# Kernel optimization log

Hardware: AMD Instinct MI355X
Metric: run time of the kernel (lower is better)

The kernel has to match this reference:

```python
import jax, jax.numpy as jnp
import numpy as np

HEAD = 16

def setup_inputs() -> dict:
    key = jax.random.key(0)
    k1, k2, k3 = jax.random.split(key, 3)
    B, S, D = 2, 2048, 1024
    x = jax.random.normal(k1, (B, S, D), dtype=jnp.float32)
    w_qkv = jax.random.normal(k2, (D, 3 * D), dtype=jnp.float32) * (1.0 / np.sqrt(D))
    b_qkv = jnp.zeros((3 * D,), dtype=jnp.float32)
    w_out = jax.random.normal(k3, (D, D), dtype=jnp.float32) * (1.0 / np.sqrt(D))
    b_out = jnp.zeros((D,), dtype=jnp.float32)
    return {"x": x, "w_qkv": w_qkv, "b_qkv": b_qkv, "w_out": w_out, "b_out": b_out}


def reference(x, w_qkv, b_qkv, w_out, b_out):
    B, S, D = x.shape
    hd = D // HEAD  # head dim
    qkv = x @ w_qkv + b_qkv                      # [B,S,3D]
    qkv = qkv.reshape(B, S, 3, HEAD, hd)
    qkv = jnp.transpose(qkv, (2, 0, 3, 1, 4))    # [3,B,H,S,hd]
    q, k, v = qkv[0], qkv[1], qkv[2]
    scores = jnp.einsum('bhqd,bhkd->bhqk', q, k)  # [B,H,S,S]
    causal = jnp.triu(jnp.ones((S, S), dtype=bool), k=1)
    scores = jnp.where(causal, -jnp.inf, scores)
    scores = scores / jnp.sqrt(jnp.asarray(hd, dtype=x.dtype))
    attn = jax.nn.softmax(scores, axis=-1)
    z = jnp.einsum('bhqk,bhkd->bhqd', attn, v)   # [B,H,S,hd]
    z = jnp.transpose(z, (0, 2, 1, 3)).reshape(B, S, D)
    out = z @ w_out + b_out
    return out
```

## Files before the change

### kernel.cpp

```cpp
#include <hip/hip_runtime.h>

#define S_LEN  2048
#define NH     16
#define HD     64
#define DMODEL 1024

using bf16x8 = __attribute__((ext_vector_type(8))) __bf16;
using f32x4  = __attribute__((ext_vector_type(4))) float;

__device__ __forceinline__ unsigned short f2bf(float f) {
    unsigned u = __float_as_uint(f);
    u += 0x7FFFu + ((u >> 16) & 1u);
    return (unsigned short)(u >> 16);
}
__device__ __forceinline__ unsigned pk_trunc(float lo, float hi) {
    return __builtin_amdgcn_perm(__float_as_uint(hi), __float_as_uint(lo), 0x07060302u);
}

#define GLDS16(gsrc, ldst) \
    __builtin_amdgcn_global_load_lds((__attribute__((address_space(1))) void*)(gsrc), \
                                     (__attribute__((address_space(3))) void*)(ldst), 16, 0, 0)

#define WAIT_LGKM0() __builtin_amdgcn_s_waitcnt(0xC07F)

__global__ __launch_bounds__(256) void prep_kernel(
    const float* __restrict__ x, const float* __restrict__ w_qkv,
    const float* __restrict__ w_out,
    unsigned short* __restrict__ xb, unsigned short* __restrict__ wqkvT,
    unsigned short* __restrict__ woutT) {
    __shared__ float T[32][33];
    int bx = blockIdx.x;
    if (bx < 4096) {
        int idx = (bx * 256 + threadIdx.x) * 4;
        float4 v = *(const float4*)(x + idx);
        ushort4 o;
        o.x = f2bf(v.x); o.y = f2bf(v.y); o.z = f2bf(v.z); o.w = f2bf(v.w);
        *(ushort4*)(xb + idx) = o;
        return;
    }
    int tb = bx - 4096;
    int tcol = tb & 127, krow = tb >> 7;
    const float* in;
    unsigned short* out;
    int N, nbx;
    if (tcol < 96) { in = w_qkv; out = wqkvT; N = 3072; nbx = tcol; }
    else           { in = w_out; out = woutT; N = 1024; nbx = tcol - 96; }
    int r  = threadIdx.x >> 3;
    int c4 = (threadIdx.x & 7) * 4;
    int kbase = krow * 32, nbase = nbx * 32;
    float4 v = *(const float4*)(in + (size_t)(kbase + r) * N + nbase + c4);
    T[r][c4 + 0] = v.x; T[r][c4 + 1] = v.y; T[r][c4 + 2] = v.z; T[r][c4 + 3] = v.w;
    __syncthreads();
    ushort4 o;
    o.x = f2bf(T[c4 + 0][r]); o.y = f2bf(T[c4 + 1][r]);
    o.z = f2bf(T[c4 + 2][r]); o.w = f2bf(T[c4 + 3][r]);
    *(ushort4*)(out + (size_t)(nbase + r) * 1024 + kbase + c4) = o;
}

template <int NI>
__device__ __forceinline__ void mfma_mainloop64(const unsigned short* __restrict__ A,
                                                const unsigned short* __restrict__ B,
                                                int K, int m0, int n0,
                                                unsigned short* As, unsigned short* Bs,
                                                f32x4 acc[4][NI]) {
    const int lane = threadIdx.x & 63, wave = threadIdx.x >> 6;
    const int quad = lane >> 4, l15 = lane & 15;
    const int wm0 = (wave >> 1) * 64, wn0 = (wave & 1) * (NI * 16);

    for (int k0 = 0; k0 < K; k0 += 64) {
        __syncthreads();
        #pragma unroll
        for (int j = 0; j < 4 + NI; ++j) {
            if (j < 4) {
                int c0 = j * 256 + wave * 64;
                int c  = c0 + lane;
                int r = c >> 3, pc = c & 7, q = pc ^ (r & 7);
                GLDS16(A + (size_t)(m0 + r) * K + k0 + q * 8, As + c0 * 8);
            } else {
                int c0 = (j - 4) * 256 + wave * 64;
                int c  = c0 + lane;
                int r = c >> 3, pc = c & 7, q = pc ^ (r & 7);
                GLDS16(B + (size_t)(n0 + r) * K + k0 + q * 8, Bs + c0 * 8);
            }
        }
        __syncthreads();

        bf16x8 af[2][4], bfr[2][NI];
        #pragma unroll
        for (int mi = 0; mi < 4; ++mi) {
            int r = wm0 + mi * 16 + l15, x = r & 7;
            af[0][mi] = *(const bf16x8*)(As + r * 64 + ((quad    ) ^ x) * 8);
            af[1][mi] = *(const bf16x8*)(As + r * 64 + ((4 + quad) ^ x) * 8);
        }
        #pragma unroll
        for (int ni = 0; ni < NI; ++ni) {
            int r = wn0 + ni * 16 + l15, x = r & 7;
            bfr[0][ni] = *(const bf16x8*)(Bs + r * 64 + ((quad    ) ^ x) * 8);
            bfr[1][ni] = *(const bf16x8*)(Bs + r * 64 + ((4 + quad) ^ x) * 8);
        }
        #pragma unroll
        for (int h = 0; h < 2; ++h)
            #pragma unroll
            for (int mi = 0; mi < 4; ++mi)
                #pragma unroll
                for (int ni = 0; ni < NI; ++ni)
                    acc[mi][ni] = __builtin_amdgcn_mfma_f32_16x16x32_bf16(
                        af[h][mi], bfr[h][ni], acc[mi][ni], 0, 0, 0);
    }
}

__global__ __launch_bounds__(256) void gemm_qkv_kernel(
    const unsigned short* __restrict__ xb, const unsigned short* __restrict__ wT,
    const float* __restrict__ bias,
    unsigned short* __restrict__ Qt, unsigned short* __restrict__ Kh,
    unsigned short* __restrict__ Vt) {
    __shared__ __align__(16) unsigned short Sh[16384];
    unsigned short* As = Sh;
    unsigned short* Bs = Sh + 8192;

    f32x4 acc[4][4];
    #pragma unroll
    for (int i = 0; i < 4; ++i)
        #pragma unroll
        for (int j = 0; j < 4; ++j) acc[i][j] = (f32x4){0.f, 0.f, 0.f, 0.f};

    const int bid = blockIdx.x;
    const int xcd = bid & 7, slot = bid >> 3;
    const int nt = xcd * 3 + (slot % 3);
    const int mt = slot / 3;
    const int m0 = mt * 128, n0 = nt * 128;
    mfma_mainloop64<4>(xb, wT, DMODEL, m0, n0, As, Bs, acc);

    const int lane = threadIdx.x & 63, wave = threadIdx.x >> 6;
    const int quad = lane >> 4, l15 = lane & 15;
    const int wm0 = (wave >> 1) * 64, wn0 = (wave & 1) * 64;

    const int colbase = n0 + wn0;
    const int t = colbase >> 10;
    const int h = (colbase >> 6) & (NH - 1);
    const float qscale = (t == 0) ? 0.125f * 1.44269504088896f : 1.0f;
    float bv[4];
    #pragma unroll
    for (int ni = 0; ni < 4; ++ni) bv[ni] = bias[colbase + ni * 16 + l15];

    __syncthreads();
    unsigned short* Lw = Sh + wave * 1536;

    #pragma unroll
    for (int mi = 0; mi < 4; ++mi) {
        int mbase = m0 + wm0 + mi * 16;
        int b = mbase >> 11, sbase = mbase & (S_LEN - 1);
        if (t == 1) {
            #pragma unroll
            for (int ni = 0; ni < 4; ++ni)
                #pragma unroll
                for (int r = 0; r < 4; ++r)
                    Lw[(quad * 4 + r) * 72 + ni * 16 + l15] =
                        f2bf(acc[mi][ni][r] + bv[ni]);
            WAIT_LGKM0();
            int rr = lane & 15, dc = (lane >> 4) * 16;
            uint4 v0 = *(const uint4*)(Lw + rr * 72 + dc);
            uint4 v1 = *(const uint4*)(Lw + rr * 72 + dc + 8);
            unsigned short* dst =
                Kh + ((size_t)(b * NH + h) * S_LEN + sbase + rr) * HD + dc;
            *(uint4*)dst = v0;
            *(uint4*)(dst + 8) = v1;
        } else {
            #pragma unroll
            for (int ni = 0; ni < 4; ++ni)
                #pragma unroll
                for (int r = 0; r < 4; ++r)
                    Lw[(ni * 16 + l15) * 24 + quad * 4 + r] =
                        f2bf((acc[mi][ni][r] + bv[ni]) * qscale);
            WAIT_LGKM0();
            int c = lane;
            uint4 v0 = *(const uint4*)(Lw + c * 24);
            uint4 v1 = *(const uint4*)(Lw + c * 24 + 8);
            unsigned short* base = (t == 0) ? Qt : Vt;
            unsigned short* dst =
                base + ((size_t)(b * NH + h) * HD + c) * S_LEN + sbase;
            *(uint4*)dst = v0;
            *(uint4*)(dst + 8) = v1;
        }
        WAIT_LGKM0();
    }
}

__global__ __launch_bounds__(256) void gemm_out_kernel(
    const unsigned short* __restrict__ zb, const unsigned short* __restrict__ wT,
    const float* __restrict__ bias, float* __restrict__ out) {
    __shared__ __align__(16) unsigned short As[8192], Bs[4096];
    f32x4 acc[4][2];
    #pragma unroll
    for (int i = 0; i < 4; ++i)
        #pragma unroll
        for (int j = 0; j < 2; ++j) acc[i][j] = (f32x4){0.f, 0.f, 0.f, 0.f};

    const int bid = blockIdx.x;
    const int xcd = bid & 7, slot = bid >> 3;
    const int nt = xcd * 2 + (slot & 1);
    const int mt = slot >> 1;
    const int m0 = mt * 128, n0 = nt * 64;
    mfma_mainloop64<2>(zb, wT, DMODEL, m0, n0, As, Bs, acc);

    const int lane = threadIdx.x & 63, wave = threadIdx.x >> 6;
    const int quad = lane >> 4, l15 = lane & 15;
    const int wm0 = (wave >> 1) * 64, wn0 = (wave & 1) * 32;
    #pragma unroll
    for (int mi = 0; mi < 4; ++mi) {
        #pragma unroll
        for (int ni = 0; ni < 2; ++ni) {
            int col = n0 + wn0 + ni * 16 + l15;
            float bvv = bias[col];
            #pragma unroll
            for (int r = 0; r < 4; ++r)
                out[(size_t)(m0 + wm0 + mi * 16 + quad * 4 + r) * DMODEL + col] =
                    acc[mi][ni][r] + bvv;
        }
    }
}

__device__ const int g_sched[47 * 4] = {
    16,0,16,-1,
    31,0,15,0,  31,16,31,1,  30,0,15,0,  15,0,15,-1,
    30,16,30,1, 29,0,14,0,   29,15,29,1, 28,0,14,0,  14,0,14,-1,
    28,15,28,1, 27,0,13,0,   27,14,27,1, 26,0,13,0,  13,0,13,-1,
    26,14,26,1, 25,0,12,0,   25,13,25,1, 24,0,12,0,  12,0,12,-1,
    24,13,24,1, 23,0,11,0,   23,12,23,1, 22,0,11,0,  11,0,11,-1,
    22,12,22,1, 21,0,10,0,   21,11,21,1, 20,0,10,0,  10,0,10,-1,
    20,11,20,1, 19,0,9,0,    19,10,19,1, 18,0,9,0,   9,0,9,-1,
    18,10,18,1, 17,0,8,0,    17,9,17,1,  8,0,8,-1,
    7,0,7,-1, 6,0,6,-1, 5,0,5,-1, 4,0,4,-1, 3,0,3,-1, 2,0,2,-1, 1,0,1,-1, 0,0,0,-1
};

__global__ __launch_bounds__(256) void attn_mfma_kernel(
    const unsigned short* __restrict__ Qt, const unsigned short* __restrict__ Kh,
    const unsigned short* __restrict__ Vt, unsigned short* __restrict__ zb,
    float* __restrict__ Zp, float* __restrict__ lp) {
    __shared__ __align__(16) unsigned short Ks[64 * 64];
    __shared__ __align__(16) unsigned short Vs[64 * 64];
    __shared__ __align__(16) unsigned short Pl[4 * 16 * 64];

    const int lane = threadIdx.x & 63, wave = threadIdx.x >> 6;
    const int quad = lane >> 4, l15 = lane & 15;
    const int bh = blockIdx.x;
    const int qt   = g_sched[blockIdx.y * 4 + 0];
    const int klo  = g_sched[blockIdx.y * 4 + 1];
    const int khi  = g_sched[blockIdx.y * 4 + 2];
    const int part = g_sched[blockIdx.y * 4 + 3];
    const int q0 = qt * 64;
    const float M0 = 12.0f;

    bf16x8 qf0, qf1;
    {
        const unsigned short* qb = Qt + (size_t)bh * HD * S_LEN + q0 + wave * 16 + l15;
        union { bf16x8 v; unsigned short u[8]; } u0, u1;
        #pragma unroll
        for (int j = 0; j < 8; ++j) {
            u0.u[j] = qb[(quad * 8 + j) * S_LEN];
            u1.u[j] = qb[(32 + quad * 8 + j) * S_LEN];
        }
        qf0 = u0.v; qf1 = u1.v;
    }

    f32x4 Z[4];
    #pragma unroll
    for (int i = 0; i < 4; ++i) Z[i] = (f32x4){0.f, 0.f, 0.f, 0.f};
    float rsum = 0.f;

    unsigned short* pw = Pl + wave * 1024;
    const int pwrow = l15 * 64;
    const int qthr  = wave * 16 + l15 - quad * 4;

    for (int kt = klo; kt <= khi; ++kt) {
        __syncthreads();
        #pragma unroll
        for (int i = 0; i < 2; ++i) {
            int c0 = (i * 4 + wave) * 64;
            int c  = c0 + lane;
            int r = c >> 3, pc = c & 7, q = pc ^ (r & 7);
            GLDS16(Kh + ((size_t)bh * S_LEN + kt * 64 + r) * HD + q * 8, Ks + c0 * 8);
        }
        #pragma unroll
        for (int i = 0; i < 2; ++i) {
            int c0 = (i * 4 + wave) * 64;
            int c  = c0 + lane;
            int d = c >> 3, pc = c & 7, q = pc ^ (d & 7);
            GLDS16(Vt + ((size_t)bh * HD + d) * S_LEN + kt * 64 + q * 8, Vs + c0 * 8);
        }
        __syncthreads();

        const bool diag = (kt == qt);
        const int nmax = diag ? wave : 3;

        #pragma unroll
        for (int n = 0; n < 4; ++n) {
            int woff = pwrow + (((2 * n + (quad >> 1)) ^ (l15 & 7)) << 3) + (quad & 1) * 4;
            if (n <= nmax) {
                int rk = n * 16 + l15;
                int x = rk & 7;
                bf16x8 kv0 = *(const bf16x8*)(Ks + rk * 64 + ((quad    ) ^ x) * 8);
                bf16x8 kv1 = *(const bf16x8*)(Ks + rk * 64 + ((4 + quad) ^ x) * 8);
                f32x4 t4 = (f32x4){-M0, -M0, -M0, -M0};
                t4 = __builtin_amdgcn_mfma_f32_16x16x32_bf16(kv0, qf0, t4, 0, 0, 0);
                t4 = __builtin_amdgcn_mfma_f32_16x16x32_bf16(kv1, qf1, t4, 0, 0, 0);
                float p[4];
                #pragma unroll
                for (int r = 0; r < 4; ++r) {
                    p[r] = exp2f(t4[r]);
                    if (diag && (n * 16 + r) > qthr) p[r] = 0.f;
                    rsum += p[r];
                }
                uint2 pk;
                pk.x = pk_trunc(p[0], p[1]);
                pk.y = pk_trunc(p[2], p[3]);
                *(uint2*)(pw + woff) = pk;
            } else {
                *(uint2*)(pw + woff) = (uint2){0u, 0u};
            }
        }

        const int khmax = diag ? (wave >> 1) : 1;
        for (int kh = 0; kh <= khmax; ++kh) {
            bf16x8 pa = *(const bf16x8*)(pw + pwrow + ((kh * 4 + quad) ^ (l15 & 7)) * 8);
            #pragma unroll
            for (int ni = 0; ni < 4; ++ni) {
                int rd = ni * 16 + l15;
                bf16x8 vb = *(const bf16x8*)(Vs + rd * 64 + ((kh * 4 + quad) ^ (rd & 7)) * 8);
                Z[ni] = __builtin_amdgcn_mfma_f32_16x16x32_bf16(vb, pa, Z[ni], 0, 0, 0);
            }
        }
    }

    rsum += __shfl_xor(rsum, 16);
    rsum += __shfl_xor(rsum, 32);

    const int ql = wave * 16 + l15;
    if (part < 0) {
        const int b = bh >> 4, h = bh & (NH - 1);
        float inv = 1.f / rsum;
        size_t rowoff = (size_t)(b * S_LEN + q0 + ql) * DMODEL + h * HD;
        #pragma unroll
        for (int ni = 0; ni < 4; ++ni) {
            ushort4 o;
            o.x = f2bf(Z[ni][0] * inv);
            o.y = f2bf(Z[ni][1] * inv);
            o.z = f2bf(Z[ni][2] * inv);
            o.w = f2bf(Z[ni][3] * inv);
            *(ushort4*)(zb + rowoff + ni * 16 + quad * 4) = o;
        }
    } else {
        const int slot = (qt - 17) * 2 + part;
        float* zpo = Zp + ((size_t)(slot * 32 + bh) * 64) * 64;
        #pragma unroll
        for (int ni = 0; ni < 4; ++ni) {
            float4 st;
            st.x = Z[ni][0]; st.y = Z[ni][1]; st.z = Z[ni][2]; st.w = Z[ni][3];
            *(float4*)(zpo + (size_t)ql * 64 + ni * 16 + quad * 4) = st;
        }
        if (quad == 0)
            lp[(size_t)(slot * 32 + bh) * 64 + ql] = rsum;
    }
}

__global__ __launch_bounds__(256) void attn_merge_kernel(
    const float* __restrict__ Zp, const float* __restrict__ lp,
    unsigned short* __restrict__ zb) {
    const int bh = blockIdx.x, qi = blockIdx.y, qt = 17 + qi;
    const int t = threadIdx.x;
    const int q = t >> 2;
    const int d0 = (t & 3) << 4;
    const int s0 = qi * 2, s1 = s0 + 1;
    float l = lp[(size_t)(s0 * 32 + bh) * 64 + q] +
              lp[(size_t)(s1 * 32 + bh) * 64 + q];
    float inv = 1.f / l;
    const float* z0 = Zp + ((size_t)(s0 * 32 + bh) * 64 + q) * 64 + d0;
    const float* z1 = Zp + ((size_t)(s1 * 32 + bh) * 64 + q) * 64 + d0;
    const int b = bh >> 4, h = bh & (NH - 1);
    unsigned short* o =
        zb + (size_t)(b * S_LEN + qt * 64 + q) * DMODEL + h * HD + d0;
    #pragma unroll
    for (int i = 0; i < 16; i += 4) {
        float4 a = *(const float4*)(z0 + i);
        float4 c = *(const float4*)(z1 + i);
        ushort4 ov;
        ov.x = f2bf((a.x + c.x) * inv);
        ov.y = f2bf((a.y + c.y) * inv);
        ov.z = f2bf((a.z + c.z) * inv);
        ov.w = f2bf((a.w + c.w) * inv);
        *(ushort4*)(o + i) = ov;
    }
}

extern "C" void kernel_launch(void* const* d_in, const int* in_sizes, int n_in,
                              void* d_out, int out_size, void* d_ws, size_t ws_size,
                              hipStream_t stream)
{
    const float* x     = (const float*)d_in[0];
    const float* w_qkv = (const float*)d_in[1];
    const float* b_qkv = (const float*)d_in[2];
    const float* w_out = (const float*)d_in[3];
    const float* b_out = (const float*)d_in[4];
    float* out = (float*)d_out;

    unsigned short* wsu   = (unsigned short*)d_ws;
    unsigned short* xb    = wsu;
    unsigned short* wqkvT = xb    + (size_t)4194304;
    unsigned short* woutT = wqkvT + (size_t)3145728;
    unsigned short* Qt    = woutT + (size_t)1048576;
    unsigned short* Kh    = Qt    + (size_t)4194304;
    unsigned short* Vt    = Kh    + (size_t)4194304;
    unsigned short* zb    = Vt    + (size_t)4194304;
    float* Zp = (float*)(zb + (size_t)4194304);
    float* lp = Zp + (size_t)30 * 32 * 64 * 64;

    prep_kernel<<<dim3(8192), 256, 0, stream>>>(x, w_qkv, w_out, xb, wqkvT, woutT);

    gemm_qkv_kernel<<<dim3(768), 256, 0, stream>>>(
        xb, wqkvT, b_qkv, Qt, Kh, Vt);

    attn_mfma_kernel<<<dim3(2 * NH, 47), 256, 0, stream>>>(Qt, Kh, Vt, zb, Zp, lp);
    attn_merge_kernel<<<dim3(2 * NH, 15), 256, 0, stream>>>(Zp, lp, zb);

    gemm_out_kernel<<<dim3(512), 256, 0, stream>>>(
        zb, woutT, b_out, out);
}
```

Baseline: 191.0 us.

## Fuse all stages into one persistent cooperative kernel with grid syncs

Replaces the five kernel launches with a single cooperative kernel of 512 blocks. It runs the prep, QKV GEMM, attention and output GEMM phases in sequence, separated by grid.sync. Attention now pairs query tiles (pi, 31-pi) per block, which balances causal work and removes the split/merge partial buffers. A new tile schedule is used for the QKV GEMM. The aim is to remove launch gaps and the merge pass, at the cost of grid-barrier overhead, fewer attention blocks (only 512, serialized loops), and a fallback to the old path if the cooperative launch fails.

```diff
diff --git a/kernel.cpp b/kernel.cpp
--- a/kernel.cpp
+++ b/kernel.cpp
@@ -1,10 +1,13 @@
 #include <hip/hip_runtime.h>
+#include <hip/hip_cooperative_groups.h>
 
 #define S_LEN  2048
 #define NH     16
 #define HD     64
 #define DMODEL 1024
 
+namespace cg = cooperative_groups;
+
 using bf16x8 = __attribute__((ext_vector_type(8))) __bf16;
 using f32x4  = __attribute__((ext_vector_type(4))) float;
 
@@ -22,6 +25,342 @@
                                      (__attribute__((address_space(3))) void*)(ldst), 16, 0, 0)
 
 #define WAIT_LGKM0() __builtin_amdgcn_s_waitcnt(0xC07F)
+
+template <int NI>
+__device__ __forceinline__ void mfma_mainloop64(const unsigned short* __restrict__ A,
+                                                const unsigned short* __restrict__ B,
+                                                int K, int m0, int n0,
+                                                unsigned short* As, unsigned short* Bs,
+                                                f32x4 acc[4][NI]) {
+    const int lane = threadIdx.x & 63, wave = threadIdx.x >> 6;
+    const int quad = lane >> 4, l15 = lane & 15;
+    const int wm0 = (wave >> 1) * 64, wn0 = (wave & 1) * (NI * 16);
+
+    for (int k0 = 0; k0 < K; k0 += 64) {
+        __syncthreads();
+        #pragma unroll
+        for (int j = 0; j < 4 + NI; ++j) {
+            if (j < 4) {
+                int c0 = j * 256 + wave * 64;
+                int c  = c0 + lane;
+                int r = c >> 3, pc = c & 7, q = pc ^ (r & 7);
+                GLDS16(A + (size_t)(m0 + r) * K + k0 + q * 8, As + c0 * 8);
+            } else {
+                int c0 = (j - 4) * 256 + wave * 64;
+                int c  = c0 + lane;
+                int r = c >> 3, pc = c & 7, q = pc ^ (r & 7);
+                GLDS16(B + (size_t)(n0 + r) * K + k0 + q * 8, Bs + c0 * 8);
+            }
+        }
+        __syncthreads();
+
+        bf16x8 af[2][4], bfr[2][NI];
+        #pragma unroll
+        for (int mi = 0; mi < 4; ++mi) {
+            int r = wm0 + mi * 16 + l15, x = r & 7;
+            af[0][mi] = *(const bf16x8*)(As + r * 64 + ((quad    ) ^ x) * 8);
+            af[1][mi] = *(const bf16x8*)(As + r * 64 + ((4 + quad) ^ x) * 8);
+        }
+        #pragma unroll
+        for (int ni = 0; ni < NI; ++ni) {
+            int r = wn0 + ni * 16 + l15, x = r & 7;
+            bfr[0][ni] = *(const bf16x8*)(Bs + r * 64 + ((quad    ) ^ x) * 8);
+            bfr[1][ni] = *(const bf16x8*)(Bs + r * 64 + ((4 + quad) ^ x) * 8);
+        }
+        #pragma unroll
+        for (int h = 0; h < 2; ++h)
+            #pragma unroll
+            for (int mi = 0; mi < 4; ++mi)
+                #pragma unroll
+                for (int ni = 0; ni < NI; ++ni)
+                    acc[mi][ni] = __builtin_amdgcn_mfma_f32_16x16x32_bf16(
+                        af[h][mi], bfr[h][ni], acc[mi][ni], 0, 0, 0);
+    }
+}
+
+__device__ __forceinline__ void qkv_epilogue(f32x4 acc[4][4], unsigned short* Sh,
+                                             int m0, int n0, const float* __restrict__ bias,
+                                             unsigned short* __restrict__ Qt,
+                                             unsigned short* __restrict__ Kh,
+                                             unsigned short* __restrict__ Vt) {
+    const int lane = threadIdx.x & 63, wave = threadIdx.x >> 6;
+    const int quad = lane >> 4, l15 = lane & 15;
+    const int wm0 = (wave >> 1) * 64, wn0 = (wave & 1) * 64;
+
+    const int colbase = n0 + wn0;
+    const int t = colbase >> 10;
+    const int h = (colbase >> 6) & (NH - 1);
+    const float qscale = (t == 0) ? 0.125f * 1.44269504088896f : 1.0f;
+    float bv[4];
+    #pragma unroll
+    for (int ni = 0; ni < 4; ++ni) bv[ni] = bias[colbase + ni * 16 + l15];
+
+    __syncthreads();
+    unsigned short* Lw = Sh + wave * 1536;
+
+    #pragma unroll
+    for (int mi = 0; mi < 4; ++mi) {
+        int mbase = m0 + wm0 + mi * 16;
+        int b = mbase >> 11, sbase = mbase & (S_LEN - 1);
+        if (t == 1) {
+            #pragma unroll
+            for (int ni = 0; ni < 4; ++ni)
+                #pragma unroll
+                for (int r = 0; r < 4; ++r)
+                    Lw[(quad * 4 + r) * 72 + ni * 16 + l15] =
+                        f2bf(acc[mi][ni][r] + bv[ni]);
+            WAIT_LGKM0();
+            int rr = lane & 15, dc = (lane >> 4) * 16;
+            uint4 v0 = *(const uint4*)(Lw + rr * 72 + dc);
+            uint4 v1 = *(const uint4*)(Lw + rr * 72 + dc + 8);
+            unsigned short* dst =
+                Kh + ((size_t)(b * NH + h) * S_LEN + sbase + rr) * HD + dc;
+            *(uint4*)dst = v0;
+            *(uint4*)(dst + 8) = v1;
+        } else {
+            #pragma unroll
+            for (int ni = 0; ni < 4; ++ni)
+                #pragma unroll
+                for (int r = 0; r < 4; ++r)
+                    Lw[(ni * 16 + l15) * 24 + quad * 4 + r] =
+                        f2bf((acc[mi][ni][r] + bv[ni]) * qscale);
+            WAIT_LGKM0();
+            int c = lane;
+            uint4 v0 = *(const uint4*)(Lw + c * 24);
+            uint4 v1 = *(const uint4*)(Lw + c * 24 + 8);
+            unsigned short* base = (t == 0) ? Qt : Vt;
+            unsigned short* dst =
+                base + ((size_t)(b * NH + h) * HD + c) * S_LEN + sbase;
+            *(uint4*)dst = v0;
+            *(uint4*)(dst + 8) = v1;
+        }
+        WAIT_LGKM0();
+    }
+}
+
+__device__ __forceinline__ void out_epilogue(f32x4 acc[4][2], int m0, int n0,
+                                             const float* __restrict__ bias,
+                                             float* __restrict__ out) {
+    const int lane = threadIdx.x & 63, wave = threadIdx.x >> 6;
+    const int quad = lane >> 4, l15 = lane & 15;
+    const int wm0 = (wave >> 1) * 64, wn0 = (wave & 1) * 32;
+    #pragma unroll
+    for (int mi = 0; mi < 4; ++mi) {
+        #pragma unroll
+        for (int ni = 0; ni < 2; ++ni) {
+            int col = n0 + wn0 + ni * 16 + l15;
+            float bvv = bias[col];
+            #pragma unroll
+            for (int r = 0; r < 4; ++r)
+                out[(size_t)(m0 + wm0 + mi * 16 + quad * 4 + r) * DMODEL + col] =
+                    acc[mi][ni][r] + bvv;
+        }
+    }
+}
+
+__global__ __launch_bounds__(256, 2) void fused_kernel(
+    const float* __restrict__ x, const float* __restrict__ w_qkv,
+    const float* __restrict__ b_qkv, const float* __restrict__ w_out,
+    const float* __restrict__ b_out, float* __restrict__ out,
+    unsigned short* __restrict__ xb, unsigned short* __restrict__ wqkvT,
+    unsigned short* __restrict__ woutT,
+    unsigned short* __restrict__ Qt, unsigned short* __restrict__ Kh,
+    unsigned short* __restrict__ Vt, unsigned short* __restrict__ zb) {
+    __shared__ __align__(16) unsigned short Sh[16384];
+    cg::grid_group grid = cg::this_grid();
+
+    const int bid  = blockIdx.x;
+    const int lane = threadIdx.x & 63, wave = threadIdx.x >> 6;
+    const int quad = lane >> 4, l15 = lane & 15;
+
+    for (int i = bid; i < 4096; i += 512) {
+        int idx = (i * 256 + threadIdx.x) * 4;
+        float4 v = *(const float4*)(x + idx);
+        ushort4 o;
+        o.x = f2bf(v.x); o.y = f2bf(v.y); o.z = f2bf(v.z); o.w = f2bf(v.w);
+        *(ushort4*)(xb + idx) = o;
+    }
+    {
+        float* T = (float*)Sh;
+        int r  = threadIdx.x >> 3;
+        int c4 = (threadIdx.x & 7) * 4;
+        for (int i = bid; i < 4096; i += 512) {
+            int tcol = i & 127, krow = i >> 7;
+            const float* in;
+            unsigned short* o;
+            int N, nbx;
+            if (tcol < 96) { in = w_qkv; o = wqkvT; N = 3072; nbx = tcol; }
+            else           { in = w_out; o = woutT; N = 1024; nbx = tcol - 96; }
+            int kbase = krow * 32, nbase = nbx * 32;
+            __syncthreads();
+            float4 v = *(const float4*)(in + (size_t)(kbase + r) * N + nbase + c4);
+            T[r * 33 + c4 + 0] = v.x; T[r * 33 + c4 + 1] = v.y;
+            T[r * 33 + c4 + 2] = v.z; T[r * 33 + c4 + 3] = v.w;
+            __syncthreads();
+            ushort4 ov;
+            ov.x = f2bf(T[(c4 + 0) * 33 + r]); ov.y = f2bf(T[(c4 + 1) * 33 + r]);
+            ov.z = f2bf(T[(c4 + 2) * 33 + r]); ov.w = f2bf(T[(c4 + 3) * 33 + r]);
+            *(ushort4*)(o + (size_t)(nbase + r) * 1024 + kbase + c4) = ov;
+        }
+    }
+    grid.sync();
+
+    {
+        int G  = bid >> 3;
+        int hG = (G & 1) ^ ((G >> 5) & 1);
+        int HG = (G <= 32) ? (G >> 1) : (16 + ((G - 31) >> 1));
+        int cum = 8 * HG + (hG ? (bid & 7) : 0);
+        int t0 = bid + cum;
+        int ntile = 1 + hG;
+        for (int ti = 0; ti < ntile; ++ti) {
+            int t = t0 + ti;
+            int nt = t % 24, mt = t / 24;
+            int m0 = mt * 128, n0 = nt * 128;
+            f32x4 acc[4][4];
+            #pragma unroll
+            for (int i = 0; i < 4; ++i)
+                #pragma unroll
+                for (int j = 0; j < 4; ++j) acc[i][j] = (f32x4){0.f, 0.f, 0.f, 0.f};
+            mfma_mainloop64<4>(xb, wqkvT, DMODEL, m0, n0, Sh, Sh + 8192, acc);
+            qkv_epilogue(acc, Sh, m0, n0, b_qkv, Qt, Kh, Vt);
+            __syncthreads();
+        }
+    }
+    grid.sync();
+
+    {
+        const int bh = bid >> 4, pi = bid & 15;
+        const int qta = pi, qtb = 31 - pi;
+        unsigned short* Ks = Sh;
+        unsigned short* Vs = Sh + 4096;
+        unsigned short* pw = Sh + 8192 + wave * 1024;
+        const int pwrow = l15 * 64;
+        const int qthr  = wave * 16 + l15 - quad * 4;
+        const float M0 = 12.0f;
+
+        bf16x8 qa0, qa1, qb0, qb1;
+        {
+            const unsigned short* qbp =
+                Qt + (size_t)bh * HD * S_LEN + qta * 64 + wave * 16 + l15;
+            union { bf16x8 v; unsigned short u[8]; } u0, u1;
+            #pragma unroll
+            for (int j = 0; j < 8; ++j) {
+                u0.u[j] = qbp[(quad * 8 + j) * S_LEN];
+                u1.u[j] = qbp[(32 + quad * 8 + j) * S_LEN];
+            }
+            qa0 = u0.v; qa1 = u1.v;
+            qbp += (qtb - qta) * 64;
+            #pragma unroll
+            for (int j = 0; j < 8; ++j) {
+                u0.u[j] = qbp[(quad * 8 + j) * S_LEN];
+                u1.u[j] = qbp[(32 + quad * 8 + j) * S_LEN];
+            }
+            qb0 = u0.v; qb1 = u1.v;
+        }
+
+        f32x4 Za[4], Zb[4];
+        #pragma unroll
+        for (int i = 0; i < 4; ++i) {
+            Za[i] = (f32x4){0.f, 0.f, 0.f, 0.f};
+            Zb[i] = (f32x4){0.f, 0.f, 0.f, 0.f};
+        }
+        float rsa = 0.f, rsb = 0.f;
+
+        auto step = [&](bf16x8 qf0, bf16x8 qf1, f32x4* Z, float& rsum, bool diag) {
+            const int nmax = diag ? wave : 3;
+            #pragma unroll
+            for (int n = 0; n < 4; ++n) {
+                int woff = pwrow + (((2 * n + (quad >> 1)) ^ (l15 & 7)) << 3) + (quad & 1) * 4;
+                if (n <= nmax) {
+                    int rk = n * 16 + l15, xk = rk & 7;
+                    bf16x8 kv0 = *(const bf16x8*)(Ks + rk * 64 + ((quad    ) ^ xk) * 8);
+                    bf16x8 kv1 = *(const bf16x8*)(Ks + rk * 64 + ((4 + quad) ^ xk) * 8);
+                    f32x4 t4 = (f32x4){-M0, -M0, -M0, -M0};
+                    t4 = __builtin_amdgcn_mfma_f32_16x16x32_bf16(kv0, qf0, t4, 0, 0, 0);
+                    t4 = __builtin_amdgcn_mfma_f32_16x16x32_bf16(kv1, qf1, t4, 0, 0, 0);
+                    float p[4];
+                    #pragma unroll
+                    for (int r = 0; r < 4; ++r) {
+                        p[r] = exp2f(t4[r]);
+                        if (diag && (n * 16 + r) > qthr) p[r] = 0.f;
+                        rsum += p[r];
+                    }
+                    uint2 pk;
+                    pk.x = pk_trunc(p[0], p[1]);
+                    pk.y = pk_trunc(p[2], p[3]);
+                    *(uint2*)(pw + woff) = pk;
+                } else {
+                    *(uint2*)(pw + woff) = (uint2){0u, 0u};
+                }
+            }
+            const int khmax = diag ? (wave >> 1) : 1;
+            for (int kh = 0; kh <= khmax; ++kh) {
+                bf16x8 pa = *(const bf16x8*)(pw + pwrow + ((kh * 4 + quad) ^ (l15 & 7)) * 8);
+                #pragma unroll
+                for (int ni = 0; ni < 4; ++ni) {
+                    int rd = ni * 16 + l15;
+                    bf16x8 vb = *(const bf16x8*)(Vs + rd * 64 + ((kh * 4 + quad) ^ (rd & 7)) * 8);
+                    Z[ni] = __builtin_amdgcn_mfma_f32_16x16x32_bf16(vb, pa, Z[ni], 0, 0, 0);
+                }
+            }
+        };
+
+        for (int kt = 0; kt <= qtb; ++kt) {
+            __syncthreads();
+            #pragma unroll
+            for (int i = 0; i < 2; ++i) {
+                int c0 = (i * 4 + wave) * 64;
+                int c  = c0 + lane;
+                int r = c >> 3, pc = c & 7, q = pc ^ (r & 7);
+                GLDS16(Kh + ((size_t)bh * S_LEN + kt * 64 + r) * HD + q * 8, Ks + c0 * 8);
+            }
+            #pragma unroll
+            for (int i = 0; i < 2; ++i) {
+                int c0 = (i * 4 + wave) * 64;
+                int c  = c0 + lane;
+                int d = c >> 3, pc = c & 7, q = pc ^ (d & 7);
+                GLDS16(Vt + ((size_t)bh * HD + d) * S_LEN + kt * 64 + q * 8, Vs + c0 * 8);
+            }
+            __syncthreads();
+
+            step(qb0, qb1, Zb, rsb, kt == qtb);
+            if (kt <= qta) step(qa0, qa1, Za, rsa, kt == qta);
+        }
+
+        const int b = bh >> 4, h = bh & (NH - 1);
+        const int ql = wave * 16 + l15;
+        auto emit = [&](int q0, f32x4* Z, float rsum) {
+            rsum += __shfl_xor(rsum, 16);
+            rsum += __shfl_xor(rsum, 32);
+            float inv = 1.f / rsum;
+            size_t rowoff = (size_t)(b * S_LEN + q0 + ql) * DMODEL + h * HD;
+            #pragma unroll
+            for (int ni = 0; ni < 4; ++ni) {
+                ushort4 o;
+                o.x = f2bf(Z[ni][0] * inv);
+                o.y = f2bf(Z[ni][1] * inv);
+                o.z = f2bf(Z[ni][2] * inv);
+                o.w = f2bf(Z[ni][3] * inv);
+                *(ushort4*)(zb + rowoff + ni * 16 + quad * 4) = o;
+            }
+        };
+        emit(qta * 64, Za, rsa);
+        emit(qtb * 64, Zb, rsb);
+    }
+    grid.sync();
+
+    {
+        int nt = bid & 15, mt = bid >> 4;
+        int m0 = mt * 128, n0 = nt * 64;
+        f32x4 acc[4][2];
+        #pragma unroll
+        for (int i = 0; i < 4; ++i)
+            #pragma unroll
+            for (int j = 0; j < 2; ++j) acc[i][j] = (f32x4){0.f, 0.f, 0.f, 0.f};
+        mfma_mainloop64<2>(zb, woutT, DMODEL, m0, n0, Sh, Sh + 8192, acc);
+        out_epilogue(acc, m0, n0, b_out, out);
+    }
+}
 
 __global__ __launch_bounds__(256) void prep_kernel(
     const float* __restrict__ x, const float* __restrict__ w_qkv,
@@ -57,133 +396,22 @@
     *(ushort4*)(out + (size_t)(nbase + r) * 1024 + kbase + c4) = o;
 }
 
-template <int NI>
-__device__ __forceinline__ void mfma_mainloop64(const unsigned short* __restrict__ A,
-                                                const unsigned short* __restrict__ B,
-                                                int K, int m0, int n0,
-                                                unsigned short* As, unsigned short* Bs,
-                                                f32x4 acc[4][NI]) {
-    const int lane = threadIdx.x & 63, wave = threadIdx.x >> 6;
-    const int quad = lane >> 4, l15 = lane & 15;
-    const int wm0 = (wave >> 1) * 64, wn0 = (wave & 1) * (NI * 16);
-
-    for (int k0 = 0; k0 < K; k0 += 64) {
-        __syncthreads();
-        #pragma unroll
-        for (int j = 0; j < 4 + NI; ++j) {
-            if (j < 4) {
-                int c0 = j * 256 + wave * 64;
-                int c  = c0 + lane;
-                int r = c >> 3, pc = c & 7, q = pc ^ (r & 7);
-                GLDS16(A + (size_t)(m0 + r) * K + k0 + q * 8, As + c0 * 8);
-            } else {
-                int c0 = (j - 4) * 256 + wave * 64;
-                int c  = c0 + lane;
-                int r = c >> 3, pc = c & 7, q = pc ^ (r & 7);
-                GLDS16(B + (size_t)(n0 + r) * K + k0 + q * 8, Bs + c0 * 8);
-            }
-        }
-        __syncthreads();
-
-        bf16x8 af[2][4], bfr[2][NI];
-        #pragma unroll
-        for (int mi = 0; mi < 4; ++mi) {
-            int r = wm0 + mi * 16 + l15, x = r & 7;
-            af[0][mi] = *(const bf16x8*)(As + r * 64 + ((quad    ) ^ x) * 8);
-            af[1][mi] = *(const bf16x8*)(As + r * 64 + ((4 + quad) ^ x) * 8);
-        }
-        #pragma unroll
-        for (int ni = 0; ni < NI; ++ni) {
-            int r = wn0 + ni * 16 + l15, x = r & 7;
-            bfr[0][ni] = *(const bf16x8*)(Bs + r * 64 + ((quad    ) ^ x) * 8);
-            bfr[1][ni] = *(const bf16x8*)(Bs + r * 64 + ((4 + quad) ^ x) * 8);
-        }
-        #pragma unroll
-        for (int h = 0; h < 2; ++h)
-            #pragma unroll
-            for (int mi = 0; mi < 4; ++mi)
-                #pragma unroll
-                for (int ni = 0; ni < NI; ++ni)
-                    acc[mi][ni] = __builtin_amdgcn_mfma_f32_16x16x32_bf16(
-                        af[h][mi], bfr[h][ni], acc[mi][ni], 0, 0, 0);
-    }
-}
-
 __global__ __launch_bounds__(256) void gemm_qkv_kernel(
     const unsigned short* __restrict__ xb, const unsigned short* __restrict__ wT,
     const float* __restrict__ bias,
     unsigned short* __restrict__ Qt, unsigned short* __restrict__ Kh,
     unsigned short* __restrict__ Vt) {
     __shared__ __align__(16) unsigned short Sh[16384];
-    unsigned short* As = Sh;
-    unsigned short* Bs = Sh + 8192;
-
     f32x4 acc[4][4];
     #pragma unroll
     for (int i = 0; i < 4; ++i)
         #pragma unroll
         for (int j = 0; j < 4; ++j) acc[i][j] = (f32x4){0.f, 0.f, 0.f, 0.f};
-
     const int bid = blockIdx.x;
-    const int xcd = bid & 7, slot = bid >> 3;
-    const int nt = xcd * 3 + (slot % 3);
-    const int mt = slot / 3;
+    const int nt = bid % 24, mt = bid / 24;
     const int m0 = mt * 128, n0 = nt * 128;
-    mfma_mainloop64<4>(xb, wT, DMODEL, m0, n0, As, Bs, acc);
-
-    const int lane = threadIdx.x & 63, wave = threadIdx.x >> 6;
-    const int quad = lane >> 4, l15 = lane & 15;
-    const int wm0 = (wave >> 1) * 64, wn0 = (wave & 1) * 64;
-
-    const int colbase = n0 + wn0;
-    const int t = colbase >> 10;
-    const int h = (colbase >> 6) & (NH - 1);
-    const float qscale = (t == 0) ? 0.125f * 1.44269504088896f : 1.0f;
-    float bv[4];
-    #pragma unroll
-    for (int ni = 0; ni < 4; ++ni) bv[ni] = bias[colbase + ni * 16 + l15];
-
-    __syncthreads();
-    unsigned short* Lw = Sh + wave * 1536;
-
-    #pragma unroll
-    for (int mi = 0; mi < 4; ++mi) {
-        int mbase = m0 + wm0 + mi * 16;
-        int b = mbase >> 11, sbase = mbase & (S_LEN - 1);
-        if (t == 1) {
-            #pragma unroll
-            for (int ni = 0; ni < 4; ++ni)
-                #pragma unroll
-                for (int r = 0; r < 4; ++r)
-                    Lw[(quad * 4 + r) * 72 + ni * 16 + l15] =
-                        f2bf(acc[mi][ni][r] + bv[ni]);
-            WAIT_LGKM0();
-            int rr = lane & 15, dc = (lane >> 4) * 16;
-            uint4 v0 = *(const uint4*)(Lw + rr * 72 + dc);
-            uint4 v1 = *(const uint4*)(Lw + rr * 72 + dc + 8);
-            unsigned short* dst =
-                Kh + ((size_t)(b * NH + h) * S_LEN + sbase + rr) * HD + dc;
-            *(uint4*)dst = v0;
-            *(uint4*)(dst + 8) = v1;
-        } else {
-            #pragma unroll
-            for (int ni = 0; ni < 4; ++ni)
-                #pragma unroll
-                for (int r = 0; r < 4; ++r)
-                    Lw[(ni * 16 + l15) * 24 + quad * 4 + r] =
-                        f2bf((acc[mi][ni][r] + bv[ni]) * qscale);
-            WAIT_LGKM0();
-            int c = lane;
-            uint4 v0 = *(const uint4*)(Lw + c * 24);
-            uint4 v1 = *(const uint4*)(Lw + c * 24 + 8);
-            unsigned short* base = (t == 0) ? Qt : Vt;
-            unsigned short* dst =
-                base + ((size_t)(b * NH + h) * HD + c) * S_LEN + sbase;
-            *(uint4*)dst = v0;
-            *(uint4*)(dst + 8) = v1;
-        }
-        WAIT_LGKM0();
-    }
+    mfma_mainloop64<4>(xb, wT, DMODEL, m0, n0, Sh, Sh + 8192, acc);
+    qkv_epilogue(acc, Sh, m0, n0, bias, Qt, Kh, Vt);
 }
 
 __global__ __launch_bounds__(256) void gemm_out_kernel(
@@ -195,29 +423,10 @@
     for (int i = 0; i < 4; ++i)
         #pragma unroll
         for (int j = 0; j < 2; ++j) acc[i][j] = (f32x4){0.f, 0.f, 0.f, 0.f};
-
-    const int bid = blockIdx.x;
-    const int xcd = bid & 7, slot = bid >> 3;
-    const int nt = xcd * 2 + (slot & 1);
-    const int mt = slot >> 1;
+    const int nt = blockIdx.x & 15, mt = blockIdx.x >> 4;
     const int m0 = mt * 128, n0 = nt * 64;
     mfma_mainloop64<2>(zb, wT, DMODEL, m0, n0, As, Bs, acc);
-
-    const int lane = threadIdx.x & 63, wave = threadIdx.x >> 6;
-    const int quad = lane >> 4, l15 = lane & 15;
-    const int wm0 = (wave >> 1) * 64, wn0 = (wave & 1) * 32;
-    #pragma unroll
-    for (int mi = 0; mi < 4; ++mi) {
-        #pragma unroll
-        for (int ni = 0; ni < 2; ++ni) {
-            int col = n0 + wn0 + ni * 16 + l15;
-            float bvv = bias[col];
-            #pragma unroll
-            for (int r = 0; r < 4; ++r)
-                out[(size_t)(m0 + wm0 + mi * 16 + quad * 4 + r) * DMODEL + col] =
-                    acc[mi][ni][r] + bvv;
-        }
-    }
+    out_epilogue(acc, m0, n0, bias, out);
 }
 
 __device__ const int g_sched[47 * 4] = {
@@ -414,14 +623,19 @@
     float* Zp = (float*)(zb + (size_t)4194304);
     float* lp = Zp + (size_t)30 * 32 * 64 * 64;
 
-    prep_kernel<<<dim3(8192), 256, 0, stream>>>(x, w_qkv, w_out, xb, wqkvT, woutT);
-
-    gemm_qkv_kernel<<<dim3(768), 256, 0, stream>>>(
-        xb, wqkvT, b_qkv, Qt, Kh, Vt);
-
-    attn_mfma_kernel<<<dim3(2 * NH, 47), 256, 0, stream>>>(Qt, Kh, Vt, zb, Zp, lp);
-    attn_merge_kernel<<<dim3(2 * NH, 15), 256, 0, stream>>>(Zp, lp, zb);
-
-    gemm_out_kernel<<<dim3(512), 256, 0, stream>>>(
-        zb, woutT, b_out, out);
-}
+    void* kargs[] = {
+        (void*)&x, (void*)&w_qkv, (void*)&b_qkv, (void*)&w_out, (void*)&b_out,
+        (void*)&out, (void*)&xb, (void*)&wqkvT, (void*)&woutT,
+        (void*)&Qt, (void*)&Kh, (void*)&Vt, (void*)&zb
+    };
+    hipError_t err = hipLaunchCooperativeKernel(
+        (const void*)fused_kernel, dim3(512), dim3(256), kargs, 0, stream);
+
+    if (err != hipSuccess) {
+        prep_kernel<<<dim3(8192), 256, 0, stream>>>(x, w_qkv, w_out, xb, wqkvT, woutT);
+        gemm_qkv_kernel<<<dim3(768), 256, 0, stream>>>(xb, wqkvT, b_qkv, Qt, Kh, Vt);
+        attn_mfma_kernel<<<dim3(2 * NH, 47), 256, 0, stream>>>(Qt, Kh, Vt, zb, Zp, lp);
+        attn_merge_kernel<<<dim3(2 * NH, 15), 256, 0, stream>>>(Zp, lp, zb);
+        gemm_out_kernel<<<dim3(512), 256, 0, stream>>>(zb, woutT, b_out, out);
+    }
+}
```

New measurement: 408.9 us. 114% more time.

## Pair causal query tiles per block, sharing K/V loads, and drop split-merge kernel

Applied to the files above, without the earlier changes.

Each block now handles two query tiles, qt and 31-qt, so every block does the same amount of causal work. The K/V tiles loaded into LDS are shared by both query tiles for the overlapping range. This replaces the 47-entry split schedule and the separate merge kernel with partial outputs, removing one launch and the fp32 partial round trip through global memory. The cost is 512 blocks with a longer serial loop each (32 K tiles), more accumulator registers per thread, and less parallelism per block than the earlier split.

```diff
diff --git a/kernel.cpp b/kernel.cpp
--- a/kernel.cpp
+++ b/kernel.cpp
@@ -220,87 +220,60 @@
     }
 }
 
-__device__ const int g_sched[47 * 4] = {
-    16,0,16,-1,
-    31,0,15,0,  31,16,31,1,  30,0,15,0,  15,0,15,-1,
-    30,16,30,1, 29,0,14,0,   29,15,29,1, 28,0,14,0,  14,0,14,-1,
-    28,15,28,1, 27,0,13,0,   27,14,27,1, 26,0,13,0,  13,0,13,-1,
-    26,14,26,1, 25,0,12,0,   25,13,25,1, 24,0,12,0,  12,0,12,-1,
-    24,13,24,1, 23,0,11,0,   23,12,23,1, 22,0,11,0,  11,0,11,-1,
-    22,12,22,1, 21,0,10,0,   21,11,21,1, 20,0,10,0,  10,0,10,-1,
-    20,11,20,1, 19,0,9,0,    19,10,19,1, 18,0,9,0,   9,0,9,-1,
-    18,10,18,1, 17,0,8,0,    17,9,17,1,  8,0,8,-1,
-    7,0,7,-1, 6,0,6,-1, 5,0,5,-1, 4,0,4,-1, 3,0,3,-1, 2,0,2,-1, 1,0,1,-1, 0,0,0,-1
-};
-
-__global__ __launch_bounds__(256) void attn_mfma_kernel(
+__global__ __launch_bounds__(256) void attn_pair_kernel(
     const unsigned short* __restrict__ Qt, const unsigned short* __restrict__ Kh,
-    const unsigned short* __restrict__ Vt, unsigned short* __restrict__ zb,
-    float* __restrict__ Zp, float* __restrict__ lp) {
-    __shared__ __align__(16) unsigned short Ks[64 * 64];
-    __shared__ __align__(16) unsigned short Vs[64 * 64];
-    __shared__ __align__(16) unsigned short Pl[4 * 16 * 64];
+    const unsigned short* __restrict__ Vt, unsigned short* __restrict__ zb) {
+    __shared__ __align__(16) unsigned short Ks[4096];
+    __shared__ __align__(16) unsigned short Vs[4096];
+    __shared__ __align__(16) unsigned short Pl[4096];
 
     const int lane = threadIdx.x & 63, wave = threadIdx.x >> 6;
     const int quad = lane >> 4, l15 = lane & 15;
-    const int bh = blockIdx.x;
-    const int qt   = g_sched[blockIdx.y * 4 + 0];
-    const int klo  = g_sched[blockIdx.y * 4 + 1];
-    const int khi  = g_sched[blockIdx.y * 4 + 2];
-    const int part = g_sched[blockIdx.y * 4 + 3];
-    const int q0 = qt * 64;
+    const int bh = blockIdx.x >> 4, pi = blockIdx.x & 15;
+    const int qta = pi, qtb = 31 - pi;
     const float M0 = 12.0f;
-
-    bf16x8 qf0, qf1;
-    {
-        const unsigned short* qb = Qt + (size_t)bh * HD * S_LEN + q0 + wave * 16 + l15;
-        union { bf16x8 v; unsigned short u[8]; } u0, u1;
-        #pragma unroll
-        for (int j = 0; j < 8; ++j) {
-            u0.u[j] = qb[(quad * 8 + j) * S_LEN];
-            u1.u[j] = qb[(32 + quad * 8 + j) * S_LEN];
-        }
-        qf0 = u0.v; qf1 = u1.v;
-    }
-
-    f32x4 Z[4];
-    #pragma unroll
-    for (int i = 0; i < 4; ++i) Z[i] = (f32x4){0.f, 0.f, 0.f, 0.f};
-    float rsum = 0.f;
 
     unsigned short* pw = Pl + wave * 1024;
     const int pwrow = l15 * 64;
     const int qthr  = wave * 16 + l15 - quad * 4;
 
-    for (int kt = klo; kt <= khi; ++kt) {
-        __syncthreads();
-        #pragma unroll
-        for (int i = 0; i < 2; ++i) {
-            int c0 = (i * 4 + wave) * 64;
-            int c  = c0 + lane;
-            int r = c >> 3, pc = c & 7, q = pc ^ (r & 7);
-            GLDS16(Kh + ((size_t)bh * S_LEN + kt * 64 + r) * HD + q * 8, Ks + c0 * 8);
-        }
-        #pragma unroll
-        for (int i = 0; i < 2; ++i) {
-            int c0 = (i * 4 + wave) * 64;
-            int c  = c0 + lane;
-            int d = c >> 3, pc = c & 7, q = pc ^ (d & 7);
-            GLDS16(Vt + ((size_t)bh * HD + d) * S_LEN + kt * 64 + q * 8, Vs + c0 * 8);
-        }
-        __syncthreads();
-
-        const bool diag = (kt == qt);
+    bf16x8 qa0, qa1, qb0, qb1;
+    {
+        const unsigned short* qbp =
+            Qt + (size_t)bh * HD * S_LEN + qta * 64 + wave * 16 + l15;
+        union { bf16x8 v; unsigned short u[8]; } u0, u1;
+        #pragma unroll
+        for (int j = 0; j < 8; ++j) {
+            u0.u[j] = qbp[(quad * 8 + j) * S_LEN];
+            u1.u[j] = qbp[(32 + quad * 8 + j) * S_LEN];
+        }
+        qa0 = u0.v; qa1 = u1.v;
+        qbp += (qtb - qta) * 64;
+        #pragma unroll
+        for (int j = 0; j < 8; ++j) {
+            u0.u[j] = qbp[(quad * 8 + j) * S_LEN];
+            u1.u[j] = qbp[(32 + quad * 8 + j) * S_LEN];
+        }
+        qb0 = u0.v; qb1 = u1.v;
+    }
+
+    f32x4 Za[4], Zb[4];
+    #pragma unroll
+    for (int i = 0; i < 4; ++i) {
+        Za[i] = (f32x4){0.f, 0.f, 0.f, 0.f};
+        Zb[i] = (f32x4){0.f, 0.f, 0.f, 0.f};
+    }
+    float rsa = 0.f, rsb = 0.f;
+
+    auto step = [&](bf16x8 qf0, bf16x8 qf1, f32x4* Z, float& rsum, bool diag) {
         const int nmax = diag ? wave : 3;
-
         #pragma unroll
         for (int n = 0; n < 4; ++n) {
             int woff = pwrow + (((2 * n + (quad >> 1)) ^ (l15 & 7)) << 3) + (quad & 1) * 4;
             if (n <= nmax) {
-                int rk = n * 16 + l15;
-                int x = rk & 7;
-                bf16x8 kv0 = *(const bf16x8*)(Ks + rk * 64 + ((quad    ) ^ x) * 8);
-                bf16x8 kv1 = *(const bf16x8*)(Ks + rk * 64 + ((4 + quad) ^ x) * 8);
+                int rk = n * 16 + l15, xk = rk & 7;
+                bf16x8 kv0 = *(const bf16x8*)(Ks + rk * 64 + ((quad    ) ^ xk) * 8);
+                bf16x8 kv1 = *(const bf16x8*)(Ks + rk * 64 + ((4 + quad) ^ xk) * 8);
                 f32x4 t4 = (f32x4){-M0, -M0, -M0, -M0};
                 t4 = __builtin_amdgcn_mfma_f32_16x16x32_bf16(kv0, qf0, t4, 0, 0, 0);
                 t4 = __builtin_amdgcn_mfma_f32_16x16x32_bf16(kv1, qf1, t4, 0, 0, 0);
@@ -319,7 +292,6 @@
                 *(uint2*)(pw + woff) = (uint2){0u, 0u};
             }
         }
-
         const int khmax = diag ? (wave >> 1) : 1;
         for (int kh = 0; kh <= khmax; ++kh) {
             bf16x8 pa = *(const bf16x8*)(pw + pwrow + ((kh * 4 + quad) ^ (l15 & 7)) * 8);
@@ -330,14 +302,35 @@
                 Z[ni] = __builtin_amdgcn_mfma_f32_16x16x32_bf16(vb, pa, Z[ni], 0, 0, 0);
             }
         }
-    }
-
-    rsum += __shfl_xor(rsum, 16);
-    rsum += __shfl_xor(rsum, 32);
-
+    };
+
+    for (int kt = 0; kt <= qtb; ++kt) {
+        __syncthreads();
+        #pragma unroll
+        for (int i = 0; i < 2; ++i) {
+            int c0 = (i * 4 + wave) * 64;
+            int c  = c0 + lane;
+            int r = c >> 3, pc = c & 7, q = pc ^ (r & 7);
+            GLDS16(Kh + ((size_t)bh * S_LEN + kt * 64 + r) * HD + q * 8, Ks + c0 * 8);
+        }
+        #pragma unroll
+        for (int i = 0; i < 2; ++i) {
+            int c0 = (i * 4 + wave) * 64;
+            int c  = c0 + lane;
+            int d = c >> 3, pc = c & 7, q = pc ^ (d & 7);
+            GLDS16(Vt + ((size_t)bh * HD + d) * S_LEN + kt * 64 + q * 8, Vs + c0 * 8);
+        }
+        __syncthreads();
+
+        step(qb0, qb1, Zb, rsb, kt == qtb);
+        if (kt <= qta) step(qa0, qa1, Za, rsa, kt == qta);
+    }
+
+    const int b = bh >> 4, h = bh & (NH - 1);
     const int ql = wave * 16 + l15;
-    if (part < 0) {
-        const int b = bh >> 4, h = bh & (NH - 1);
+    auto emit = [&](int q0, f32x4* Z, float rsum) {
+        rsum += __shfl_xor(rsum, 16);
+        rsum += __shfl_xor(rsum, 32);
         float inv = 1.f / rsum;
         size_t rowoff = (size_t)(b * S_LEN + q0 + ql) * DMODEL + h * HD;
         #pragma unroll
@@ -349,47 +342,9 @@
             o.w = f2bf(Z[ni][3] * inv);
             *(ushort4*)(zb + rowoff + ni * 16 + quad * 4) = o;
         }
-    } else {
-        const int slot = (qt - 17) * 2 + part;
-        float* zpo = Zp + ((size_t)(slot * 32 + bh) * 64) * 64;
-        #pragma unroll
-        for (int ni = 0; ni < 4; ++ni) {
-            float4 st;
-            st.x = Z[ni][0]; st.y = Z[ni][1]; st.z = Z[ni][2]; st.w = Z[ni][3];
-            *(float4*)(zpo + (size_t)ql * 64 + ni * 16 + quad * 4) = st;
-        }
-        if (quad == 0)
-            lp[(size_t)(slot * 32 + bh) * 64 + ql] = rsum;
-    }
-}
-
-__global__ __launch_bounds__(256) void attn_merge_kernel(
-    const float* __restrict__ Zp, const float* __restrict__ lp,
-    unsigned short* __restrict__ zb) {
-    const int bh = blockIdx.x, qi = blockIdx.y, qt = 17 + qi;
-    const int t = threadIdx.x;
-    const int q = t >> 2;
-    const int d0 = (t & 3) << 4;
-    const int s0 = qi * 2, s1 = s0 + 1;
-    float l = lp[(size_t)(s0 * 32 + bh) * 64 + q] +
-              lp[(size_t)(s1 * 32 + bh) * 64 + q];
-    float inv = 1.f / l;
-    const float* z0 = Zp + ((size_t)(s0 * 32 + bh) * 64 + q) * 64 + d0;
-    const float* z1 = Zp + ((size_t)(s1 * 32 + bh) * 64 + q) * 64 + d0;
-    const int b = bh >> 4, h = bh & (NH - 1);
-    unsigned short* o =
-        zb + (size_t)(b * S_LEN + qt * 64 + q) * DMODEL + h * HD + d0;
-    #pragma unroll
-    for (int i = 0; i < 16; i += 4) {
-        float4 a = *(const float4*)(z0 + i);
-        float4 c = *(const float4*)(z1 + i);
-        ushort4 ov;
-        ov.x = f2bf((a.x + c.x) * inv);
-        ov.y = f2bf((a.y + c.y) * inv);
-        ov.z = f2bf((a.z + c.z) * inv);
-        ov.w = f2bf((a.w + c.w) * inv);
-        *(ushort4*)(o + i) = ov;
-    }
+    };
+    emit(qta * 64, Za, rsa);
+    emit(qtb * 64, Zb, rsb);
 }
 
 extern "C" void kernel_launch(void* const* d_in, const int* in_sizes, int n_in,
@@ -411,16 +366,13 @@
     unsigned short* Kh    = Qt    + (size_t)4194304;
     unsigned short* Vt    = Kh    + (size_t)4194304;
     unsigned short* zb    = Vt    + (size_t)4194304;
-    float* Zp = (float*)(zb + (size_t)4194304);
-    float* lp = Zp + (size_t)30 * 32 * 64 * 64;
 
     prep_kernel<<<dim3(8192), 256, 0, stream>>>(x, w_qkv, w_out, xb, wqkvT, woutT);
 
     gemm_qkv_kernel<<<dim3(768), 256, 0, stream>>>(
         xb, wqkvT, b_qkv, Qt, Kh, Vt);
 
-    attn_mfma_kernel<<<dim3(2 * NH, 47), 256, 0, stream>>>(Qt, Kh, Vt, zb, Zp, lp);
-    attn_merge_kernel<<<dim3(2 * NH, 15), 256, 0, stream>>>(Zp, lp, zb);
+    attn_pair_kernel<<<dim3(512), 256, 0, stream>>>(Qt, Kh, Vt, zb);
 
     gemm_out_kernel<<<dim3(512), 256, 0, stream>>>(
         zb, woutT, b_out, out);
```

New measurement: 203.0 us. +6.3%, slower.
